# Kernel tuning notes

Hardware: AMD Instinct MI355X
Metric: run time of the kernel (lower is better)

## Reference

```python
import jax, jax.numpy as jnp
import numpy as np

NU, NM, E, L, B = 16000, 8000, 64, 3, 100000


def setup_inputs() -> dict:
    key = jax.random.key(0)
    ks = jax.random.split(key, 10)
    # adjacency scaled small so 3 layers of propagation stay numerically tame
    user_adj = jax.random.uniform(ks[0], (NU, NM), jnp.float32) * 1e-3
    movie_adj = jax.random.uniform(ks[1], (NM, NU), jnp.float32) * 1e-3
    user_emb = jax.random.normal(ks[2], (NU, E), jnp.float32)
    movie_emb = jax.random.normal(ks[3], (NM, E), jnp.float32)
    Wu = jax.random.normal(ks[4], (L, E, E), jnp.float32) * 0.05
    bu = jnp.zeros((L, E), jnp.float32)
    Wm = jax.random.normal(ks[5], (L, E, E), jnp.float32) * 0.05
    bm = jnp.zeros((L, E), jnp.float32)
    Wo = jax.random.normal(ks[6], (1, (L + 1) * E), jnp.float32) * 0.05
    bo = jnp.zeros((1,), jnp.float32)
    user_id = jax.random.randint(ks[7], (B,), 0, NU, dtype=jnp.int32)
    movie_id = jax.random.randint(ks[8], (B,), 0, NM, dtype=jnp.int32)
    return {"user_adj": user_adj, "movie_adj": movie_adj,
            "user_emb": user_emb, "movie_emb": movie_emb,
            "Wu": Wu, "bu": bu, "Wm": Wm, "bm": bm,
            "Wo": Wo, "bo": bo,
            "user_id": user_id, "movie_id": movie_id}


def reference(user_adj, movie_adj, user_emb, movie_emb, Wu, bu, Wm, bm, Wo, bo, user_id, movie_id):
    us = [user_emb]   # [NU, E] per layer
    ms = [movie_emb]  # [NM, E] per layer
    for l in range(Wu.shape[0]):
        # layer(adj @ m) + layer(u)  ==  (adj @ m + u) @ W.T + 2*b  (bias applied twice in original)
        u = jax.nn.leaky_relu((user_adj @ ms[-1] + us[-1]) @ Wu[l].T + 2.0 * bu[l], 0.01)
        m = jax.nn.leaky_relu((movie_adj @ us[-1] + ms[-1]) @ Wm[l].T + 2.0 * bm[l], 0.01)
        us.append(u)
        ms.append(m)
    # gather-by-id elementwise multiply, concat over layers -> [B, (L+1)*E]
    inter = jnp.concatenate([u[user_id] * m[movie_id] for u, m in zip(us, ms)], axis=1)
    # dropout is identity at inference (training=False)
    out = inter @ Wo.T + bo  # [B, 1]
    return out.reshape(-1)
```

## Files before the change

kernel.cpp:

```cpp
#include <hip/hip_runtime.h>
#include <hip/hip_bf16.h>
#include <stdint.h>

#define NUQ 16000
#define NMQ 8000
#define EQ  64
#define LQ  3
#define BQ  100000

#define SPLIT 5
#define MOVIE_BLOCKS (125 * SPLIT)
#define USER_BLOCKS  (250 * SPLIT)
#define GEMM_BLOCKS  (MOVIE_BLOCKS + USER_BLOCKS)

typedef short short8 __attribute__((ext_vector_type(8)));
typedef float f32x4  __attribute__((ext_vector_type(4)));
typedef unsigned short ushort_t;

static __device__ __forceinline__ unsigned int bf16_bits(float f) {
    unsigned int u = __float_as_uint(f);
    return (u + 0x7FFFu + ((u >> 16) & 1u)) >> 16;
}
static __device__ __forceinline__ unsigned int pk_bf16(float a, float b) {
    return (bf16_bits(a) & 0xFFFFu) | (bf16_bits(b) << 16);
}

__global__ __launch_bounds__(256) void prep_kernel(
    const float* __restrict__ uemb, const float* __restrict__ memb,
    ushort_t* __restrict__ uT, ushort_t* __restrict__ mT)
{
    __shared__ float xs[64 * 65];
    int bid = blockIdx.x, t = threadIdx.x;
    bool mside = bid >= 250;
    int k0 = (mside ? (bid - 250) : bid) * 64;
    int ld = mside ? NMQ : NUQ;
    const float* src = mside ? memb : uemb;
    ushort_t* dst = mside ? mT : uT;

    for (int j = 0; j < 16; j++) {
        int idx = j * 256 + t;
        int r = idx >> 6, e = idx & 63;
        xs[r * 65 + e] = src[(size_t)(k0 + r) * 64 + e];
    }
    __syncthreads();
    for (int j = 0; j < 16; j++) {
        int idx = j * 256 + t;
        int e = idx >> 6, rr = idx & 63;
        dst[(size_t)e * ld + k0 + rr] = (ushort_t)bf16_bits(xs[rr * 65 + e]);
    }
}

template <int MODE>
__global__ __launch_bounds__(256) void gemm_kernel(
    const float* __restrict__ adjU, const float* __restrict__ adjM,
    ushort_t* __restrict__ adjUb, ushort_t* __restrict__ adjMb,
    const ushort_t* __restrict__ mT, const ushort_t* __restrict__ uT,
    float* __restrict__ tmp_u, float* __restrict__ tmp_m)
{
    __shared__ ushort_t Ash[64 * 72];
    __shared__ ushort_t Bsh[64 * 72];

    int bid = blockIdx.x, t = threadIdx.x;
    bool movie = bid < MOVIE_BLOCKS;
    int tt = movie ? bid : bid - MOVIE_BLOCKS;
    int mt = tt / SPLIT, ch = tt - mt * SPLIT;
    int M0 = mt * 64;
    int ldK = movie ? NUQ : NMQ;
    int KC  = movie ? (NUQ / SPLIT) : (NMQ / SPLIT);
    int K0  = ch * KC;
    const float* A = movie ? adjM : adjU;
    ushort_t* Ab = movie ? adjMb : adjUb;
    const ushort_t* BT = movie ? uT : mT;
    float* outp = movie ? (tmp_m + ((size_t)ch * NMQ + M0) * 64)
                        : (tmp_u + ((size_t)ch * NUQ + M0) * 64);

    int srow = t >> 2;
    int scol = (t & 3) * 16;
    size_t arow = (size_t)(M0 + srow) * ldK;
    size_t brow = (size_t)srow * ldK;

    int lane = t & 63, w = t >> 6;
    int R0 = w * 16, mrow = lane & 15, q = lane >> 4;
    const ushort_t* a_base = &Ash[(R0 + mrow) * 72 + q * 8];
    const ushort_t* b_base = &Bsh[mrow * 72 + q * 8];

    f32x4 acc[4];
#pragma unroll
    for (int nb = 0; nb < 4; nb++) acc[nb] = (f32x4){0.f, 0.f, 0.f, 0.f};

    for (int kk = K0; kk < K0 + KC; kk += 64) {
        if (MODE == 2) {
            const uint4* src = (const uint4*)(Ab + arow + kk + scol);
            uint4 q0 = src[0], q1 = src[1];
            *(uint4*)&Ash[srow * 72 + scol] = q0;
            *(uint4*)&Ash[srow * 72 + scol + 8] = q1;
        } else {
            const float4* fp = (const float4*)(A + arow + kk + scol);
            float4 f0 = fp[0], f1 = fp[1], f2 = fp[2], f3 = fp[3];
            uint4 q0, q1;
            q0.x = pk_bf16(f0.x, f0.y); q0.y = pk_bf16(f0.z, f0.w);
            q0.z = pk_bf16(f1.x, f1.y); q0.w = pk_bf16(f1.z, f1.w);
            q1.x = pk_bf16(f2.x, f2.y); q1.y = pk_bf16(f2.z, f2.w);
            q1.z = pk_bf16(f3.x, f3.y); q1.w = pk_bf16(f3.z, f3.w);
            *(uint4*)&Ash[srow * 72 + scol] = q0;
            *(uint4*)&Ash[srow * 72 + scol + 8] = q1;
            if (MODE == 1) {
                uint4* d = (uint4*)(Ab + arow + kk + scol);
                d[0] = q0; d[1] = q1;
            }
        }
        {
            const uint4* src = (const uint4*)(BT + brow + kk + scol);
            uint4 q0 = src[0], q1 = src[1];
            *(uint4*)&Bsh[srow * 72 + scol] = q0;
            *(uint4*)&Bsh[srow * 72 + scol + 8] = q1;
        }
        __syncthreads();
#pragma unroll
        for (int ks = 0; ks < 2; ks++) {
            short8 a = *(const short8*)(a_base + ks * 32);
#pragma unroll
            for (int nb = 0; nb < 4; nb++) {
                short8 b = *(const short8*)(b_base + nb * 16 * 72 + ks * 32);
                acc[nb] = __builtin_amdgcn_mfma_f32_16x16x32_bf16(a, b, acc[nb], 0, 0, 0);
            }
        }
        __syncthreads();
    }
#pragma unroll
    for (int nb = 0; nb < 4; nb++)
#pragma unroll
        for (int r = 0; r < 4; r++)
            outp[(size_t)(R0 + q * 4 + r) * 64 + nb * 16 + mrow] = acc[nb][r];
}

__global__ __launch_bounds__(256) void transform_kernel(
    const float* __restrict__ tmp_u, const float* __restrict__ tmp_m,
    const float* __restrict__ prev_u, const float* __restrict__ prev_m,
    const float* __restrict__ Wu, const float* __restrict__ bu,
    const float* __restrict__ Wm, const float* __restrict__ bm,
    float* __restrict__ out_u, float* __restrict__ out_m,
    ushort_t* __restrict__ uT, ushort_t* __restrict__ mT)
{
    __shared__ float xs[64 * 65];
    __shared__ float Ws[64 * 65];
    __shared__ float ys[64 * 65];
    int bid = blockIdx.x, t = threadIdx.x;
    bool mside = bid >= 250;
    int row0 = (mside ? (bid - 250) : bid) * 64;
    int Nrows = mside ? NMQ : NUQ;
    const float* tmp  = mside ? tmp_m : tmp_u;
    const float* prev = mside ? prev_m : prev_u;
    const float* W    = mside ? Wm : Wu;
    const float* bias = mside ? bm : bu;
    float* outp   = mside ? out_m : out_u;
    ushort_t* outT = mside ? mT : uT;

    for (int j = 0; j < 16; j++) {
        int idx = j * 256 + t;
        int r = idx >> 6, e = idx & 63;
        size_t g = (size_t)(row0 + r) * 64 + e;
        float v = prev[g];
#pragma unroll
        for (int s = 0; s < SPLIT; s++) v += tmp[(size_t)s * Nrows * 64 + g];
        xs[r * 65 + e] = v;
        Ws[r * 65 + e] = W[idx];
    }
    __syncthreads();

    int ep = t & 63, rb = t >> 6;
    float acc[16];
    float b2 = 2.0f * bias[ep];
#pragma unroll
    for (int j = 0; j < 16; j++) acc[j] = b2;
    for (int e = 0; e < 64; e++) {
        float w = Ws[ep * 65 + e];
#pragma unroll
        for (int j = 0; j < 16; j++) acc[j] += xs[(j * 4 + rb) * 65 + e] * w;
    }
#pragma unroll
    for (int j = 0; j < 16; j++) {
        float v = acc[j];
        v = v > 0.f ? v : 0.01f * v;
        ys[(j * 4 + rb) * 65 + ep] = v;
    }
    __syncthreads();

    for (int j = 0; j < 16; j++) {
        int idx = j * 256 + t;
        int r = idx >> 6, e = idx & 63;
        outp[(size_t)(row0 + r) * 64 + e] = ys[r * 65 + e];
        int e2 = r, rr = e;
        outT[(size_t)e2 * Nrows + row0 + rr] = (ushort_t)bf16_bits(ys[rr * 65 + e2]);
    }
}

__global__ __launch_bounds__(256) void gather_kernel(
    const float* __restrict__ u0, const float* __restrict__ u1,
    const float* __restrict__ u2, const float* __restrict__ u3,
    const float* __restrict__ m0, const float* __restrict__ m1,
    const float* __restrict__ m2, const float* __restrict__ m3,
    const float* __restrict__ Wo, const float* __restrict__ bo,
    const int* __restrict__ uid, const int* __restrict__ mid,
    float* __restrict__ out)
{
    int t = threadIdx.x;
    int lane = t & 63, wv = t >> 6;
    int b = blockIdx.x * 4 + wv;
    size_t ui = (size_t)uid[b] * 64 + lane;
    size_t mi = (size_t)mid[b] * 64 + lane;
    float acc = u0[ui] * m0[mi] * Wo[lane]
              + u1[ui] * m1[mi] * Wo[64 + lane]
              + u2[ui] * m2[mi] * Wo[128 + lane]
              + u3[ui] * m3[mi] * Wo[192 + lane];
#pragma unroll
    for (int off = 32; off >= 1; off >>= 1) acc += __shfl_xor(acc, off, 64);
    if (lane == 0) out[b] = acc + bo[0];
}

extern "C" void kernel_launch(void* const* d_in, const int* in_sizes, int n_in,
                              void* d_out, int out_size, void* d_ws, size_t ws_size,
                              hipStream_t stream)
{
    const float* adjU = (const float*)d_in[0];
    const float* adjM = (const float*)d_in[1];
    const float* uemb = (const float*)d_in[2];
    const float* memb = (const float*)d_in[3];
    const float* Wu   = (const float*)d_in[4];
    const float* bu   = (const float*)d_in[5];
    const float* Wm   = (const float*)d_in[6];
    const float* bm   = (const float*)d_in[7];
    const float* Wo   = (const float*)d_in[8];
    const float* bo   = (const float*)d_in[9];
    const int* uid    = (const int*)d_in[10];
    const int* mid    = (const int*)d_in[11];
    float* out = (float*)d_out;

    char* ws = (char*)d_ws;
    size_t off = 0;
    auto alloc = [&](size_t bytes) -> void* {
        void* p = ws + off;
        off += (bytes + 255) & ~(size_t)255;
        return p;
    };
    float* u_ws = (float*)alloc((size_t)3 * NUQ * 64 * 4);
    float* m_ws = (float*)alloc((size_t)3 * NMQ * 64 * 4);
    ushort_t* uT = (ushort_t*)alloc((size_t)64 * NUQ * 2);
    ushort_t* mT = (ushort_t*)alloc((size_t)64 * NMQ * 2);
    float* tmp_u = (float*)alloc((size_t)SPLIT * NUQ * 64 * 4);
    float* tmp_m = (float*)alloc((size_t)SPLIT * NMQ * 64 * 4);
    ushort_t* adjUb = (ushort_t*)alloc((size_t)NUQ * NMQ * 2);
    ushort_t* adjMb = (ushort_t*)alloc((size_t)NMQ * NUQ * 2);
    bool compress = (ws_size >= off);
    if (!compress) { adjUb = nullptr; adjMb = nullptr; }

    prep_kernel<<<375, 256, 0, stream>>>(uemb, memb, uT, mT);

    for (int l = 0; l < LQ; l++) {
        if (compress) {
            if (l == 0)
                gemm_kernel<1><<<GEMM_BLOCKS, 256, 0, stream>>>(adjU, adjM, adjUb, adjMb, mT, uT, tmp_u, tmp_m);
            else
                gemm_kernel<2><<<GEMM_BLOCKS, 256, 0, stream>>>(adjU, adjM, adjUb, adjMb, mT, uT, tmp_u, tmp_m);
        } else {
            gemm_kernel<0><<<GEMM_BLOCKS, 256, 0, stream>>>(adjU, adjM, adjUb, adjMb, mT, uT, tmp_u, tmp_m);
        }
        const float* pu = (l == 0) ? uemb : (u_ws + (size_t)(l - 1) * NUQ * 64);
        const float* pm = (l == 0) ? memb : (m_ws + (size_t)(l - 1) * NMQ * 64);
        transform_kernel<<<375, 256, 0, stream>>>(
            tmp_u, tmp_m, pu, pm,
            Wu + (size_t)l * 64 * 64, bu + (size_t)l * 64,
            Wm + (size_t)l * 64 * 64, bm + (size_t)l * 64,
            u_ws + (size_t)l * NUQ * 64, m_ws + (size_t)l * NMQ * 64,
            uT, mT);
    }

    gather_kernel<<<BQ / 4, 256, 0, stream>>>(
        uemb, u_ws, u_ws + (size_t)NUQ * 64, u_ws + (size_t)2 * NUQ * 64,
        memb, m_ws, m_ws + (size_t)NMQ * 64, m_ws + (size_t)2 * NMQ * 64,
        Wo, bo, uid, mid, out);
}
```

Baseline: 1.455 ms.

## Load GEMM operands directly from global into MFMA registers, dropping LDS staging

The adjacency GEMM kernel no longer stages A and B tiles through shared memory with barriers. Each lane now loads its MFMA fragment directly from global memory in 32-wide K steps. This removes LDS writes, reads and __syncthreads, but B fragments are re-read by all four waves. Global access also becomes strided per lane, 16 bytes per row, instead of coalesced 64-element rows.

Result: slower. 2.161 ms (+48.5%).

```diff
diff --git a/kernel.cpp b/kernel.cpp
--- a/kernel.cpp
+++ b/kernel.cpp
@@ -57,9 +57,6 @@
     const ushort_t* __restrict__ mT, const ushort_t* __restrict__ uT,
     float* __restrict__ tmp_u, float* __restrict__ tmp_m)
 {
-    __shared__ ushort_t Ash[64 * 72];
-    __shared__ ushort_t Bsh[64 * 72];
-
     int bid = blockIdx.x, t = threadIdx.x;
     bool movie = bid < MOVIE_BLOCKS;
     int tt = movie ? bid : bid - MOVIE_BLOCKS;
@@ -74,59 +71,47 @@
     float* outp = movie ? (tmp_m + ((size_t)ch * NMQ + M0) * 64)
                         : (tmp_u + ((size_t)ch * NUQ + M0) * 64);
 
-    int srow = t >> 2;
-    int scol = (t & 3) * 16;
-    size_t arow = (size_t)(M0 + srow) * ldK;
-    size_t brow = (size_t)srow * ldK;
-
-    int lane = t & 63, w = t >> 6;
-    int R0 = w * 16, mrow = lane & 15, q = lane >> 4;
-    const ushort_t* a_base = &Ash[(R0 + mrow) * 72 + q * 8];
-    const ushort_t* b_base = &Bsh[mrow * 72 + q * 8];
+    int lane = t & 63, wv = t >> 6;
+    int mrow = lane & 15, q = lane >> 4;
+    int arow = M0 + wv * 16 + mrow;
+
+    const ushort_t* aB = Ab ? (Ab + (size_t)arow * ldK + K0 + q * 8) : nullptr;
+    ushort_t*       aW = Ab ? (Ab + (size_t)arow * ldK + K0 + q * 8) : nullptr;
+    const float*    aF = A + (size_t)arow * ldK + K0 + q * 8;
+    const ushort_t* b0 = BT + (size_t)(0 * 16 + mrow) * ldK + K0 + q * 8;
+    const ushort_t* b1 = BT + (size_t)(1 * 16 + mrow) * ldK + K0 + q * 8;
+    const ushort_t* b2 = BT + (size_t)(2 * 16 + mrow) * ldK + K0 + q * 8;
+    const ushort_t* b3 = BT + (size_t)(3 * 16 + mrow) * ldK + K0 + q * 8;
 
     f32x4 acc[4];
 #pragma unroll
     for (int nb = 0; nb < 4; nb++) acc[nb] = (f32x4){0.f, 0.f, 0.f, 0.f};
 
-    for (int kk = K0; kk < K0 + KC; kk += 64) {
+#pragma unroll 2
+    for (int kk = 0; kk < KC; kk += 32) {
+        short8 a;
         if (MODE == 2) {
-            const uint4* src = (const uint4*)(Ab + arow + kk + scol);
-            uint4 q0 = src[0], q1 = src[1];
-            *(uint4*)&Ash[srow * 72 + scol] = q0;
-            *(uint4*)&Ash[srow * 72 + scol + 8] = q1;
+            a = *(const short8*)(aB + kk);
         } else {
-            const float4* fp = (const float4*)(A + arow + kk + scol);
-            float4 f0 = fp[0], f1 = fp[1], f2 = fp[2], f3 = fp[3];
-            uint4 q0, q1;
-            q0.x = pk_bf16(f0.x, f0.y); q0.y = pk_bf16(f0.z, f0.w);
-            q0.z = pk_bf16(f1.x, f1.y); q0.w = pk_bf16(f1.z, f1.w);
-            q1.x = pk_bf16(f2.x, f2.y); q1.y = pk_bf16(f2.z, f2.w);
-            q1.z = pk_bf16(f3.x, f3.y); q1.w = pk_bf16(f3.z, f3.w);
-            *(uint4*)&Ash[srow * 72 + scol] = q0;
-            *(uint4*)&Ash[srow * 72 + scol + 8] = q1;
-            if (MODE == 1) {
-                uint4* d = (uint4*)(Ab + arow + kk + scol);
-                d[0] = q0; d[1] = q1;
-            }
+            float4 f0 = *(const float4*)(aF + kk);
+            float4 f1 = *(const float4*)(aF + kk + 4);
+            uint4 qv;
+            qv.x = pk_bf16(f0.x, f0.y); qv.y = pk_bf16(f0.z, f0.w);
+            qv.z = pk_bf16(f1.x, f1.y); qv.w = pk_bf16(f1.z, f1.w);
+            a = *(const short8*)&qv;
+            if (MODE == 1) *(uint4*)(aW + kk) = qv;
         }
-        {
-            const uint4* src = (const uint4*)(BT + brow + kk + scol);
-            uint4 q0 = src[0], q1 = src[1];
-            *(uint4*)&Bsh[srow * 72 + scol] = q0;
-            *(uint4*)&Bsh[srow * 72 + scol + 8] = q1;
-        }
-        __syncthreads();
-#pragma unroll
-        for (int ks = 0; ks < 2; ks++) {
-            short8 a = *(const short8*)(a_base + ks * 32);
-#pragma unroll
-            for (int nb = 0; nb < 4; nb++) {
-                short8 b = *(const short8*)(b_base + nb * 16 * 72 + ks * 32);
-                acc[nb] = __builtin_amdgcn_mfma_f32_16x16x32_bf16(a, b, acc[nb], 0, 0, 0);
-            }
-        }
-        __syncthreads();
-    }
+        short8 vb0 = *(const short8*)(b0 + kk);
+        short8 vb1 = *(const short8*)(b1 + kk);
+        short8 vb2 = *(const short8*)(b2 + kk);
+        short8 vb3 = *(const short8*)(b3 + kk);
+        acc[0] = __builtin_amdgcn_mfma_f32_16x16x32_bf16(a, vb0, acc[0], 0, 0, 0);
+        acc[1] = __builtin_amdgcn_mfma_f32_16x16x32_bf16(a, vb1, acc[1], 0, 0, 0);
+        acc[2] = __builtin_amdgcn_mfma_f32_16x16x32_bf16(a, vb2, acc[2], 0, 0, 0);
+        acc[3] = __builtin_amdgcn_mfma_f32_16x16x32_bf16(a, vb3, acc[3], 0, 0, 0);
+    }
+
+    int R0 = wv * 16;
 #pragma unroll
     for (int nb = 0; nb < 4; nb++)
 #pragma unroll
```

## Stream bf16 adjacency via direct global-to-LDS loads with double buffering

Applied to the files above, without the earlier changes.

Adds a separate convert kernel that casts both adjacency matrices to bf16 up front, replacing the layer-0 convert-and-store inside the GEMM. A new GEMM kernel loads the bf16 adjacency and embedding tiles straight into LDS with global_load_lds, using an XOR-swizzled layout and two buffers so the next tile's loads overlap the current tile's MFMAs. The aim is to hide memory latency and drop register staging in this bandwidth-bound propagation. The cost is an extra full pass over the fp32 adjacency in a standalone kernel, and it depends on hand-placed waitcnt and barrier ordering being correct.

After: 1.512 ms. +3.9%, slower.

```diff
diff --git a/kernel.cpp b/kernel.cpp
--- a/kernel.cpp
+++ b/kernel.cpp
@@ -23,6 +23,12 @@
 }
 static __device__ __forceinline__ unsigned int pk_bf16(float a, float b) {
     return (bf16_bits(a) & 0xFFFFu) | (bf16_bits(b) << 16);
+}
+
+static __device__ __forceinline__ void glds16(const ushort_t* g, ushort_t* l) {
+    __builtin_amdgcn_global_load_lds(
+        (const __attribute__((address_space(1))) void*)g,
+        (__attribute__((address_space(3))) void*)l, 16, 0, 0);
 }
 
 __global__ __launch_bounds__(256) void prep_kernel(
@@ -50,10 +56,109 @@
     }
 }
 
-template <int MODE>
-__global__ __launch_bounds__(256) void gemm_kernel(
+__global__ __launch_bounds__(256) void convert_kernel(
+    const float* __restrict__ src, ushort_t* __restrict__ dst, long n)
+{
+    long i = (long)blockIdx.x * 256 + threadIdx.x;
+    long stride = (long)gridDim.x * 256;
+    for (; i * 8 < n; i += stride) {
+        float4 f0 = *(const float4*)(src + i * 8);
+        float4 f1 = *(const float4*)(src + i * 8 + 4);
+        uint4 q;
+        q.x = pk_bf16(f0.x, f0.y); q.y = pk_bf16(f0.z, f0.w);
+        q.z = pk_bf16(f1.x, f1.y); q.w = pk_bf16(f1.z, f1.w);
+        *(uint4*)(dst + i * 8) = q;
+    }
+}
+
+__global__ __launch_bounds__(256) void gemm_stream(
+    const ushort_t* __restrict__ adjUb, const ushort_t* __restrict__ adjMb,
+    const ushort_t* __restrict__ mT, const ushort_t* __restrict__ uT,
+    float* __restrict__ tmp_u, float* __restrict__ tmp_m)
+{
+    __shared__ ushort_t As[2 * 64 * 64];
+    __shared__ ushort_t Bs[2 * 64 * 64];
+
+    int bid = blockIdx.x, t = threadIdx.x;
+    bool movie = bid < MOVIE_BLOCKS;
+    int tt = movie ? bid : bid - MOVIE_BLOCKS;
+    int mt = tt / SPLIT, ch = tt - mt * SPLIT;
+    int M0 = mt * 64;
+    int ldK = movie ? NUQ : NMQ;
+    int KC  = movie ? (NUQ / SPLIT) : (NMQ / SPLIT);
+    int K0  = ch * KC;
+    const ushort_t* Ab = movie ? adjMb : adjUb;
+    const ushort_t* BT = movie ? uT : mT;
+    float* outp = movie ? (tmp_m + ((size_t)ch * NMQ + M0) * 64)
+                        : (tmp_u + ((size_t)ch * NUQ + M0) * 64);
+
+    int lane = t & 63, w = t >> 6;
+    int W16 = w * 16;
+
+    int lr = lane >> 3;
+    int lc = (lane & 7) ^ lr;
+    const ushort_t* aSrc0 = Ab + (size_t)(M0 + W16 + 0 + lr) * ldK + K0 + lc * 8;
+    const ushort_t* aSrc1 = Ab + (size_t)(M0 + W16 + 8 + lr) * ldK + K0 + lc * 8;
+    const ushort_t* bSrc0 = BT + (size_t)(W16 + 0 + lr) * ldK + K0 + lc * 8;
+    const ushort_t* bSrc1 = BT + (size_t)(W16 + 8 + lr) * ldK + K0 + lc * 8;
+
+    int mrow = lane & 15, q = lane >> 4;
+    int s3 = mrow & 7;
+    int cswz = (q ^ s3) * 8;
+
+    f32x4 acc[4];
+#pragma unroll
+    for (int nb = 0; nb < 4; nb++) acc[nb] = (f32x4){0.f, 0.f, 0.f, 0.f};
+
+    int NT = KC >> 6;
+
+#define STAGE_TILE(buf, kofs)                                   \
+    do {                                                        \
+        ushort_t* ab = As + (buf) * 4096 + W16 * 64;            \
+        ushort_t* bb = Bs + (buf) * 4096 + W16 * 64;            \
+        glds16(aSrc0 + (kofs), ab);                             \
+        glds16(aSrc1 + (kofs), ab + 512);                       \
+        glds16(bSrc0 + (kofs), bb);                             \
+        glds16(bSrc1 + (kofs), bb + 512);                       \
+    } while (0)
+
+    STAGE_TILE(0, 0);
+
+    for (int it = 0; it < NT; ++it) {
+        if (it + 1 < NT) {
+            STAGE_TILE((it + 1) & 1, (it + 1) * 64);
+            asm volatile("s_waitcnt vmcnt(4)" ::: "memory");
+        } else {
+            asm volatile("s_waitcnt vmcnt(0)" ::: "memory");
+        }
+        __builtin_amdgcn_s_barrier();
+
+        const ushort_t* aB = As + (it & 1) * 4096;
+        const ushort_t* bB = Bs + (it & 1) * 4096;
+#pragma unroll
+        for (int ks = 0; ks < 2; ks++) {
+            int ck = (cswz ^ (ks * 32));
+            short8 a = *(const short8*)(aB + (W16 + mrow) * 64 + ck);
+#pragma unroll
+            for (int nb = 0; nb < 4; nb++) {
+                short8 b = *(const short8*)(bB + (nb * 16 + mrow) * 64 + ck);
+                acc[nb] = __builtin_amdgcn_mfma_f32_16x16x32_bf16(a, b, acc[nb], 0, 0, 0);
+            }
+        }
+        asm volatile("" ::: "memory");
+        __builtin_amdgcn_s_barrier();
+    }
+#undef STAGE_TILE
+
+#pragma unroll
+    for (int nb = 0; nb < 4; nb++)
+#pragma unroll
+        for (int r = 0; r < 4; r++)
+            outp[(size_t)(W16 + q * 4 + r) * 64 + nb * 16 + mrow] = acc[nb][r];
+}
+
+__global__ __launch_bounds__(256) void gemm_f32(
     const float* __restrict__ adjU, const float* __restrict__ adjM,
-    ushort_t* __restrict__ adjUb, ushort_t* __restrict__ adjMb,
     const ushort_t* __restrict__ mT, const ushort_t* __restrict__ uT,
     float* __restrict__ tmp_u, float* __restrict__ tmp_m)
 {
@@ -69,7 +174,6 @@
     int KC  = movie ? (NUQ / SPLIT) : (NMQ / SPLIT);
     int K0  = ch * KC;
     const float* A = movie ? adjM : adjU;
-    ushort_t* Ab = movie ? adjMb : adjUb;
     const ushort_t* BT = movie ? uT : mT;
     float* outp = movie ? (tmp_m + ((size_t)ch * NMQ + M0) * 64)
                         : (tmp_u + ((size_t)ch * NUQ + M0) * 64);
@@ -89,31 +193,20 @@
     for (int nb = 0; nb < 4; nb++) acc[nb] = (f32x4){0.f, 0.f, 0.f, 0.f};
 
     for (int kk = K0; kk < K0 + KC; kk += 64) {
-        if (MODE == 2) {
-            const uint4* src = (const uint4*)(Ab + arow + kk + scol);
-            uint4 q0 = src[0], q1 = src[1];
-            *(uint4*)&Ash[srow * 72 + scol] = q0;
-            *(uint4*)&Ash[srow * 72 + scol + 8] = q1;
-        } else {
-            const float4* fp = (const float4*)(A + arow + kk + scol);
-            float4 f0 = fp[0], f1 = fp[1], f2 = fp[2], f3 = fp[3];
-            uint4 q0, q1;
-            q0.x = pk_bf16(f0.x, f0.y); q0.y = pk_bf16(f0.z, f0.w);
-            q0.z = pk_bf16(f1.x, f1.y); q0.w = pk_bf16(f1.z, f1.w);
-            q1.x = pk_bf16(f2.x, f2.y); q1.y = pk_bf16(f2.z, f2.w);
-            q1.z = pk_bf16(f3.x, f3.y); q1.w = pk_bf16(f3.z, f3.w);
-            *(uint4*)&Ash[srow * 72 + scol] = q0;
-            *(uint4*)&Ash[srow * 72 + scol + 8] = q1;
-            if (MODE == 1) {
-                uint4* d = (uint4*)(Ab + arow + kk + scol);
-                d[0] = q0; d[1] = q1;
-            }
-        }
+        const float4* fp = (const float4*)(A + arow + kk + scol);
+        float4 f0 = fp[0], f1 = fp[1], f2 = fp[2], f3 = fp[3];
+        uint4 q0, q1;
+        q0.x = pk_bf16(f0.x, f0.y); q0.y = pk_bf16(f0.z, f0.w);
+        q0.z = pk_bf16(f1.x, f1.y); q0.w = pk_bf16(f1.z, f1.w);
+        q1.x = pk_bf16(f2.x, f2.y); q1.y = pk_bf16(f2.z, f2.w);
+        q1.z = pk_bf16(f3.x, f3.y); q1.w = pk_bf16(f3.z, f3.w);
+        *(uint4*)&Ash[srow * 72 + scol] = q0;
+        *(uint4*)&Ash[srow * 72 + scol + 8] = q1;
         {
             const uint4* src = (const uint4*)(BT + brow + kk + scol);
-            uint4 q0 = src[0], q1 = src[1];
-            *(uint4*)&Bsh[srow * 72 + scol] = q0;
-            *(uint4*)&Bsh[srow * 72 + scol + 8] = q1;
+            uint4 b0 = src[0], b1 = src[1];
+            *(uint4*)&Bsh[srow * 72 + scol] = b0;
+            *(uint4*)&Bsh[srow * 72 + scol + 8] = b1;
         }
         __syncthreads();
 #pragma unroll
@@ -252,19 +345,18 @@
     ushort_t* adjUb = (ushort_t*)alloc((size_t)NUQ * NMQ * 2);
     ushort_t* adjMb = (ushort_t*)alloc((size_t)NMQ * NUQ * 2);
     bool compress = (ws_size >= off);
-    if (!compress) { adjUb = nullptr; adjMb = nullptr; }
 
     prep_kernel<<<375, 256, 0, stream>>>(uemb, memb, uT, mT);
+    if (compress) {
+        convert_kernel<<<2048, 256, 0, stream>>>(adjU, adjUb, (long)NUQ * NMQ);
+        convert_kernel<<<2048, 256, 0, stream>>>(adjM, adjMb, (long)NMQ * NUQ);
+    }
 
     for (int l = 0; l < LQ; l++) {
-        if (compress) {
-            if (l == 0)
-                gemm_kernel<1><<<GEMM_BLOCKS, 256, 0, stream>>>(adjU, adjM, adjUb, adjMb, mT, uT, tmp_u, tmp_m);
-            else
-                gemm_kernel<2><<<GEMM_BLOCKS, 256, 0, stream>>>(adjU, adjM, adjUb, adjMb, mT, uT, tmp_u, tmp_m);
-        } else {
-            gemm_kernel<0><<<GEMM_BLOCKS, 256, 0, stream>>>(adjU, adjM, adjUb, adjMb, mT, uT, tmp_u, tmp_m);
-        }
+        if (compress)
+            gemm_stream<<<GEMM_BLOCKS, 256, 0, stream>>>(adjUb, adjMb, mT, uT, tmp_u, tmp_m);
+        else
+            gemm_f32<<<GEMM_BLOCKS, 256, 0, stream>>>(adjU, adjM, mT, uT, tmp_u, tmp_m);
         const float* pu = (l == 0) ? uemb : (u_ws + (size_t)(l - 1) * NUQ * 64);
         const float* pm = (l == 0) ? memb : (m_ws + (size_t)(l - 1) * NMQ * 64);
         transform_kernel<<<375, 256, 0, stream>>>(
```
